# Performance work log

Hardware: AMD Instinct MI355X
Metric: run time of the kernel (lower is better)

Reference implementation:

```python
import jax, jax.numpy as jnp
import numpy as np

B, HF, WF = 16, 32, 32
DIM, NH = 1024, 16
HD = DIM // NH  # 64


def axial_freqs(H, W, head_dim):
    # RotaryEmbedding(dim=head_dim//4, freqs_for='pixel', max_freq=H*W)
    d = head_dim // 4  # rotary dim per axis
    base = jnp.linspace(1.0, (H * W) / 2.0, d // 2) * jnp.pi  # [d//2]
    posH = jnp.linspace(-1.0, 1.0, H)
    posW = jnp.linspace(-1.0, 1.0, W)
    fH = jnp.repeat(posH[:, None] * base[None, :], 2, axis=-1)  # [H, d]
    fW = jnp.repeat(posW[:, None] * base[None, :], 2, axis=-1)  # [W, d]
    fH = jnp.broadcast_to(fH[:, None, :], (H, W, d))
    fW = jnp.broadcast_to(fW[None, :, :], (H, W, d))
    return jnp.concatenate([fH, fW], axis=-1)  # [H, W, 2d] = [H, W, head_dim//2]


def rotate_half(x):
    # interleaved pair rotation: (x1, x2) -> (-x2, x1)
    xr = x.reshape(*x.shape[:-1], -1, 2)
    x1, x2 = xr[..., 0], xr[..., 1]
    return jnp.stack([-x2, x1], axis=-1).reshape(x.shape)


def apply_rotary(freqs, t):
    # t: [B, h, H, W, hd]; freqs: [H, W, rot_dim]
    rd = freqs.shape[-1]
    t_rot, t_pass = t[..., :rd], t[..., rd:]
    t_rot = t_rot * jnp.cos(freqs) + rotate_half(t_rot) * jnp.sin(freqs)
    return jnp.concatenate([t_rot, t_pass], axis=-1)


def setup_inputs() -> dict:
    key = jax.random.key(0)
    k1, k2, k3 = jax.random.split(key, 3)
    s = 1.0 / np.sqrt(DIM)
    return {
        "x": jax.random.normal(k1, (B, HF * WF, DIM), jnp.float32),
        "w_qkv": jax.random.normal(k2, (3 * DIM, DIM), jnp.float32) * s,
        "w_proj": jax.random.normal(k3, (DIM, DIM), jnp.float32) * s,
        "b_proj": jnp.zeros((DIM,), jnp.float32),
    }


def reference(x, w_qkv, w_proj, b_proj):
    freqs = axial_freqs(HF, WF, HD)
    qkv = x @ w_qkv.T  # [B, N, 3*DIM]
    q, k, v = jnp.split(qkv, 3, axis=-1)

    def to_grid(t):  # [B, N, DIM] -> [B, h, H, W, hd]
        return t.reshape(B, HF, WF, NH, HD).transpose(0, 3, 1, 2, 4)

    q, k, v = to_grid(q), to_grid(k), to_grid(v)
    q = apply_rotary(freqs, q)
    k = apply_rotary(freqs, k)
    N = HF * WF
    q = q.reshape(B, NH, N, HD)
    k = k.reshape(B, NH, N, HD)
    v = v.reshape(B, NH, N, HD)

    scale = 1.0 / np.sqrt(HD)
    attn = jax.nn.softmax(jnp.einsum('bhnd,bhmd->bhnm', q, k) * scale, axis=-1)
    out = jnp.einsum('bhnm,bhmd->bhnd', attn, v)  # [B, h, N, hd]
    out = out.transpose(0, 2, 1, 3).reshape(B, N, DIM)
    return out @ w_proj.T + b_proj
```

## Files before the change

kernel.cpp:

```cpp
#include <hip/hip_runtime.h>
#include <hip/hip_bf16.h>
#include <math.h>

typedef __bf16 bf16;
typedef bf16 bf16x4 __attribute__((ext_vector_type(4)));
typedef bf16 bf16x8 __attribute__((ext_vector_type(8)));
typedef float f32x4 __attribute__((ext_vector_type(4)));

#define MFMA16(a, b, c) __builtin_amdgcn_mfma_f32_16x16x32_bf16((a), (b), (c), 0, 0, 0)

#define QSCALE 0.18033688011112042f

__device__ __forceinline__ void async16(const void* g, void* l) {
  __builtin_amdgcn_global_load_lds(
      (const __attribute__((address_space(1))) void*)g,
      (__attribute__((address_space(3))) void*)l, 16, 0, 0);
}

__global__ __launch_bounds__(256) void f2b_all_kernel(const float* __restrict__ x,
                                                      const float* __restrict__ wqkv,
                                                      const float* __restrict__ wproj,
                                                      bf16* __restrict__ xb,
                                                      bf16* __restrict__ wqb,
                                                      bf16* __restrict__ wpb) {
  int t = blockIdx.x * 256 + threadIdx.x;
  const float* in;
  bf16* out;
  int i;
  if (t < 4194304) {
    in = x; out = xb; i = t * 4;
  } else if (t < 4980736) {
    in = wqkv; out = wqb; i = (t - 4194304) * 4;
  } else {
    in = wproj; out = wpb; i = (t - 4980736) * 4;
  }
  f32x4 v = *(const f32x4*)(in + i);
  bf16x4 o = {(bf16)v[0], (bf16)v[1], (bf16)v[2], (bf16)v[3]};
  *(bf16x4*)(out + i) = o;
}

__global__ __launch_bounds__(256) void table_kernel(float* __restrict__ cosT,
                                                    float* __restrict__ sinT) {
  int idx = blockIdx.x * 256 + threadIdx.x;
  if (idx >= 1024 * 32) return;
  int n = idx >> 5, d = idx & 31;
  int hf = n >> 5, wf = n & 31;
  int bi = (d & 15) >> 1;
  float base = (1.0f + 73.0f * bi) * 3.14159265358979323846f;
  int p = (d < 16) ? hf : wf;
  float pos = (2.0f * (float)p - 31.0f) * (1.0f / 31.0f);
  float f = pos * base;
  cosT[idx] = cosf(f);
  sinT[idx] = sinf(f);
}

template <int EPI, int NBN>
__global__ __launch_bounds__(512, 2) void gemm_bt(
    const bf16* __restrict__ A, const bf16* __restrict__ W,
    bf16* __restrict__ oq, bf16* __restrict__ okk, bf16* __restrict__ ovt,
    const float* __restrict__ cosT, const float* __restrict__ sinT,
    float* __restrict__ outF, const float* __restrict__ bias) {
  constexpr int K = 1024;
  __shared__ bf16 As[4][256 * 32];
  __shared__ bf16 Bs[4][256 * 32];

  const int tid = threadIdx.x;
  const int lane = tid & 63;
  const int wid = tid >> 6;
  const int lo = lane & 15, hi = lane >> 4;
  const int wm = wid >> 2;
  const int wn = wid & 3;

  const int wg = blockIdx.x;
  const int xcd = wg & 7;
  const int i = wg >> 3;
  const int s = i >> 4;
  const int r = i & 15;
  const int bm = xcd * 8 + (s & 1) * 4 + (r & 3);
  const int bn = (s >> 1) * 4 + (r >> 2);

  const bf16* Ab = A + (size_t)bm * 256 * K;
  const bf16* Wb = W + (size_t)bn * 256 * K;

  const f32x4 fzero = {0.f, 0.f, 0.f, 0.f};
  f32x4 acc[8][4];
#pragma unroll
  for (int i2 = 0; i2 < 8; ++i2)
#pragma unroll
    for (int j = 0; j < 4; ++j) acc[i2][j] = fzero;

  size_t srcOff[2];
  int ldsOff[2];
#pragma unroll
  for (int i2 = 0; i2 < 2; ++i2) {
    const int c = i2 * 512 + tid;
    const int row = c >> 2, g = c & 3;
    const int gsrc = g ^ ((row >> 1) & 3);
    srcOff[i2] = (size_t)row * K + gsrc * 8;
    ldsOff[i2] = c * 8;
  }

  auto stageSlot = [&](int slot, int kh) {
#pragma unroll
    for (int i2 = 0; i2 < 2; ++i2)
      async16(Ab + srcOff[i2] + kh * 32, &As[slot][ldsOff[i2]]);
#pragma unroll
    for (int i2 = 0; i2 < 2; ++i2)
      async16(Wb + srcOff[i2] + kh * 32, &Bs[slot][ldsOff[i2]]);
  };

  auto compute = [&](int slot) {
    bf16x8 af[8], bf[4];
#pragma unroll
    for (int mf = 0; mf < 8; ++mf) {
      const int row = wm * 128 + mf * 16 + lo;
      const int g = hi ^ ((row >> 1) & 3);
      af[mf] = *(const bf16x8*)&As[slot][row * 32 + g * 8];
    }
#pragma unroll
    for (int nf = 0; nf < 4; ++nf) {
      const int row = wn * 64 + nf * 16 + lo;
      const int g = hi ^ ((row >> 1) & 3);
      bf[nf] = *(const bf16x8*)&Bs[slot][row * 32 + g * 8];
    }
    __builtin_amdgcn_s_setprio(1);
#pragma unroll
    for (int mf = 0; mf < 8; ++mf)
#pragma unroll
      for (int nf = 0; nf < 4; ++nf)
        acc[mf][nf] = MFMA16(af[mf], bf[nf], acc[mf][nf]);
    __builtin_amdgcn_s_setprio(0);
  };

  stageSlot(0, 0);
  stageSlot(1, 1);

  for (int kt = 0; kt < 7; ++kt) {
#pragma unroll
    for (int ph = 0; ph < 4; ++ph) {
      stageSlot((ph + 2) & 3, kt * 4 + ph + 2);
      asm volatile("s_waitcnt vmcnt(8)" ::: "memory");
      __builtin_amdgcn_s_barrier();
      compute(ph);
    }
  }
  stageSlot(2, 30);
  asm volatile("s_waitcnt vmcnt(8)" ::: "memory");
  __builtin_amdgcn_s_barrier();
  compute(0);
  stageSlot(3, 31);
  asm volatile("s_waitcnt vmcnt(8)" ::: "memory");
  __builtin_amdgcn_s_barrier();
  compute(1);
  asm volatile("s_waitcnt vmcnt(4)" ::: "memory");
  __builtin_amdgcn_s_barrier();
  compute(2);
  asm volatile("s_waitcnt vmcnt(0)" ::: "memory");
  __builtin_amdgcn_s_barrier();
  compute(3);

  const int rb0 = bm * 256 + wm * 128;
  const int jb0 = bn * 256 + wn * 64;

  if constexpr (EPI == 0) {
#pragma unroll
    for (int ac = 0; ac < 4; ++ac) {
      const int j = jb0 + ac * 16 + lo;
      const int which = j >> 10;
      const int f = j & 1023;
      const int h = f >> 6, d = f & 63;
#pragma unroll
      for (int ar = 0; ar < 8; ++ar) {
        const int rb = rb0 + ar * 16 + 4 * hi;
        f32x4 v = acc[ar][ac];
        if (which == 2) {
          const int b = rb >> 10, n0 = rb & 1023;
          bf16x4 pk = {(bf16)v[0], (bf16)v[1], (bf16)v[2], (bf16)v[3]};
          *(bf16x4*)(ovt + ((size_t)((b * 16 + h) * 64 + d)) * 1024 + n0) = pk;
        } else {
          bf16* dst = which ? okk : oq;
          const float sc = which ? 1.0f : QSCALE;
#pragma unroll
          for (int reg = 0; reg < 4; ++reg) {
            const int r2 = rb + reg;
            const int b = r2 >> 10, n = r2 & 1023;
            float val = v[reg];
            float res;
            if (d < 32) {
              float c = cosT[n * 32 + d];
              float sn = sinT[n * 32 + d];
              float pp = __shfl_xor(val, 1);
              res = (d & 1) ? fmaf(val, c, pp * sn) : fmaf(val, c, -(pp * sn));
            } else {
              res = val;
            }
            dst[((size_t)((b * 16 + h) * 1024 + n)) * 64 + d] = (bf16)(res * sc);
          }
        }
      }
    }
  } else {
#pragma unroll
    for (int ac = 0; ac < 4; ++ac) {
      const int j = jb0 + ac * 16 + lo;
      const float bv = bias[j];
#pragma unroll
      for (int ar = 0; ar < 8; ++ar) {
        const int rb = rb0 + ar * 16 + 4 * hi;
#pragma unroll
        for (int reg = 0; reg < 4; ++reg)
          outF[(size_t)(rb + reg) * 1024 + j] = acc[ar][ac][reg] + bv;
      }
    }
  }
}

__global__ __launch_bounds__(512, 4) void attn_fwd(const bf16* __restrict__ q,
                                                   const bf16* __restrict__ k,
                                                   const bf16* __restrict__ vt,
                                                   bf16* __restrict__ o) {
  __shared__ bf16 Kt[2][64 * 64];
  __shared__ bf16 Vt[2][64 * 64];
  __shared__ bf16 Pt[8][32 * 68];
  const int tid = threadIdx.x;
  const int lane = tid & 63, wid = tid >> 6;
  const int lo = lane & 15, hi = lane >> 4;
  const int j = blockIdx.x;
  const int bh = (j & 7) + ((j >> 5) << 3);
  const int qt = (j >> 3) & 3;
  const bf16* qg = q + (size_t)bh * 65536;
  const bf16* kg = k + (size_t)bh * 65536;
  const bf16* vg = vt + (size_t)bh * 65536;

  bf16x8 qf[2][2];
#pragma unroll
  for (int rg = 0; rg < 2; ++rg) {
    const int qrow = qt * 256 + wid * 32 + rg * 16 + lo;
#pragma unroll
    for (int ch = 0; ch < 2; ++ch)
      qf[rg][ch] = *(const bf16x8*)(qg + (size_t)qrow * 64 + ch * 32 + 8 * hi);
  }

  const int srow = tid >> 3;
  const int sgsrc = (tid & 7) ^ (srow & 7);
  auto stageKV = [&](int buf, int kv) {
    async16(kg + (size_t)(kv * 64 + srow) * 64 + sgsrc * 8, &Kt[buf][tid * 8]);
    async16(vg + (size_t)srow * 1024 + kv * 64 + sgsrc * 8, &Vt[buf][tid * 8]);
  };

  asm volatile("s_waitcnt vmcnt(0)" ::: "memory");
  stageKV(0, 0);

  const f32x4 fzero = {0.f, 0.f, 0.f, 0.f};
  f32x4 of[2][4];
  float psum[2][4];
#pragma unroll
  for (int rg = 0; rg < 2; ++rg)
#pragma unroll
    for (int r = 0; r < 4; ++r) {
      of[rg][r] = fzero;
      psum[rg][r] = 0.f;
    }

  const int m7 = lo & 7;

  for (int kv = 0; kv < 16; ++kv) {
    const int cur = kv & 1;
    if (kv < 15) {
      stageKV(cur ^ 1, kv + 1);
      asm volatile("s_waitcnt vmcnt(2)" ::: "memory");
    } else {
      asm volatile("s_waitcnt vmcnt(0)" ::: "memory");
    }
    __builtin_amdgcn_s_barrier();

#pragma unroll
    for (int kf = 0; kf < 4; ++kf) {
      const int r = kf * 16 + lo;
      bf16x8 kb0 = *(const bf16x8*)&Kt[cur][r * 64 + ((hi ^ m7) * 8)];
      bf16x8 kb1 = *(const bf16x8*)&Kt[cur][r * 64 + (((hi + 4) ^ m7) * 8)];
#pragma unroll
      for (int rg = 0; rg < 2; ++rg) {
        f32x4 z = fzero;
        z = MFMA16(qf[rg][0], kb0, z);
        z = MFMA16(qf[rg][1], kb1, z);
#pragma unroll
        for (int reg = 0; reg < 4; ++reg) {
          float p = __builtin_amdgcn_exp2f(z[reg]);
          psum[rg][reg] += p;
          Pt[wid][(rg * 16 + 4 * hi + reg) * 68 + kf * 16 + lo] = (bf16)p;
        }
      }
    }

    bf16x8 pa[2][2];
#pragma unroll
    for (int rg = 0; rg < 2; ++rg)
#pragma unroll
      for (int ch = 0; ch < 2; ++ch)
        pa[rg][ch] = *(const bf16x8*)&Pt[wid][(rg * 16 + lo) * 68 + ch * 32 + 8 * hi];
#pragma unroll
    for (int df = 0; df < 4; ++df) {
      const int r = df * 16 + lo;
      bf16x8 vb0 = *(const bf16x8*)&Vt[cur][r * 64 + ((hi ^ m7) * 8)];
      bf16x8 vb1 = *(const bf16x8*)&Vt[cur][r * 64 + (((hi + 4) ^ m7) * 8)];
#pragma unroll
      for (int rg = 0; rg < 2; ++rg) {
        of[rg][df] = MFMA16(pa[rg][0], vb0, of[rg][df]);
        of[rg][df] = MFMA16(pa[rg][1], vb1, of[rg][df]);
      }
    }
    __syncthreads();
  }

#pragma unroll
  for (int off = 1; off < 16; off <<= 1) {
#pragma unroll
    for (int rg = 0; rg < 2; ++rg)
#pragma unroll
      for (int reg = 0; reg < 4; ++reg) psum[rg][reg] += __shfl_xor(psum[rg][reg], off);
  }

  const int b = bh >> 4, h = bh & 15;
#pragma unroll
  for (int rg = 0; rg < 2; ++rg)
#pragma unroll
    for (int reg = 0; reg < 4; ++reg) {
      const int n = qt * 256 + wid * 32 + rg * 16 + 4 * hi + reg;
      const float inv = 1.0f / psum[rg][reg];
#pragma unroll
      for (int df = 0; df < 4; ++df)
        o[((size_t)(b * 1024 + n)) * 1024 + h * 64 + df * 16 + lo] =
            (bf16)(of[rg][df][reg] * inv);
    }
}

extern "C" void kernel_launch(void* const* d_in, const int* in_sizes, int n_in,
                              void* d_out, int out_size, void* d_ws, size_t ws_size,
                              hipStream_t stream) {
  (void)in_sizes; (void)n_in; (void)out_size; (void)ws_size;
  const float* x = (const float*)d_in[0];
  const float* wqkv = (const float*)d_in[1];
  const float* wproj = (const float*)d_in[2];
  const float* bproj = (const float*)d_in[3];

  char* ws = (char*)d_ws;
  bf16* xb = (bf16*)(ws);
  bf16* wqb = (bf16*)(ws + 33554432);
  bf16* wpb = (bf16*)(ws + 39845888);
  float* cosT = (float*)(ws + 41943040);
  float* sinT = (float*)(ws + 42074112);
  bf16* qb = (bf16*)(ws + 42205184);
  bf16* kb = (bf16*)(ws + 75759616);
  bf16* vtb = (bf16*)(ws + 109314048);

  f2b_all_kernel<<<20480, 256, 0, stream>>>(x, wqkv, wproj, xb, wqb, wpb);
  table_kernel<<<128, 256, 0, stream>>>(cosT, sinT);

  gemm_bt<0, 12><<<768, 512, 0, stream>>>(xb, wqb, qb, kb, vtb, cosT, sinT,
                                          nullptr, nullptr);
  attn_fwd<<<1024, 512, 0, stream>>>(qb, kb, vtb, xb);
  gemm_bt<1, 4><<<256, 512, 0, stream>>>(xb, wpb, nullptr, nullptr, nullptr,
                                         nullptr, nullptr, (float*)d_out, bproj);
}
```

Baseline: 273.2 us.

## Switch attention to 32x32x16 MFMA and keep P in registers via permlane swap

```diff
diff --git a/kernel.cpp b/kernel.cpp
--- a/kernel.cpp
+++ b/kernel.cpp
@@ -3,11 +3,16 @@
 #include <math.h>
 
 typedef __bf16 bf16;
+typedef bf16 bf16x2 __attribute__((ext_vector_type(2)));
 typedef bf16 bf16x4 __attribute__((ext_vector_type(4)));
 typedef bf16 bf16x8 __attribute__((ext_vector_type(8)));
 typedef float f32x4 __attribute__((ext_vector_type(4)));
+typedef float f32x16 __attribute__((ext_vector_type(16)));
+typedef unsigned int uint;
+typedef uint uint32x4 __attribute__((ext_vector_type(4)));
 
 #define MFMA16(a, b, c) __builtin_amdgcn_mfma_f32_16x16x32_bf16((a), (b), (c), 0, 0, 0)
+#define MFMA32(a, b, c) __builtin_amdgcn_mfma_f32_32x32x16_bf16((a), (b), (c), 0, 0, 0)
 
 #define QSCALE 0.18033688011112042f
 
@@ -15,6 +20,15 @@
   __builtin_amdgcn_global_load_lds(
       (const __attribute__((address_space(1))) void*)g,
       (__attribute__((address_space(3))) void*)l, 16, 0, 0);
+}
+
+__device__ __forceinline__ uint pkbf(float a, float b) {
+  bf16x2 t = {(bf16)a, (bf16)b};
+  return __builtin_bit_cast(uint, t);
+}
+
+__device__ __forceinline__ void pls(uint& x, uint& y) {
+  asm volatile("v_permlane32_swap_b32 %0, %1" : "+v"(x), "+v"(y));
 }
 
 __global__ __launch_bounds__(256) void f2b_all_kernel(const float* __restrict__ x,
@@ -221,10 +235,12 @@
                                                    bf16* __restrict__ o) {
   __shared__ bf16 Kt[2][64 * 64];
   __shared__ bf16 Vt[2][64 * 64];
-  __shared__ bf16 Pt[8][32 * 68];
+  __shared__ float Psm[8][32];
   const int tid = threadIdx.x;
   const int lane = tid & 63, wid = tid >> 6;
-  const int lo = lane & 15, hi = lane >> 4;
+  const int l31 = lane & 31;
+  const int s = lane >> 5;
+  const int m7 = l31 & 7;
   const int j = blockIdx.x;
   const int bh = (j & 7) + ((j >> 5) << 3);
   const int qt = (j >> 3) & 3;
@@ -232,14 +248,11 @@
   const bf16* kg = k + (size_t)bh * 65536;
   const bf16* vg = vt + (size_t)bh * 65536;
 
-  bf16x8 qf[2][2];
-#pragma unroll
-  for (int rg = 0; rg < 2; ++rg) {
-    const int qrow = qt * 256 + wid * 32 + rg * 16 + lo;
-#pragma unroll
-    for (int ch = 0; ch < 2; ++ch)
-      qf[rg][ch] = *(const bf16x8*)(qg + (size_t)qrow * 64 + ch * 32 + 8 * hi);
-  }
+  const int qrow = qt * 256 + wid * 32 + l31;
+  bf16x8 qf[4];
+#pragma unroll
+  for (int kb4 = 0; kb4 < 4; ++kb4)
+    qf[kb4] = *(const bf16x8*)(qg + (size_t)qrow * 64 + kb4 * 16 + s * 8);
 
   const int srow = tid >> 3;
   const int sgsrc = (tid & 7) ^ (srow & 7);
@@ -251,18 +264,10 @@
   asm volatile("s_waitcnt vmcnt(0)" ::: "memory");
   stageKV(0, 0);
 
-  const f32x4 fzero = {0.f, 0.f, 0.f, 0.f};
-  f32x4 of[2][4];
-  float psum[2][4];
-#pragma unroll
-  for (int rg = 0; rg < 2; ++rg)
-#pragma unroll
-    for (int r = 0; r < 4; ++r) {
-      of[rg][r] = fzero;
-      psum[rg][r] = 0.f;
-    }
-
-  const int m7 = lo & 7;
+  f32x16 of0 = {0.f, 0.f, 0.f, 0.f, 0.f, 0.f, 0.f, 0.f,
+                0.f, 0.f, 0.f, 0.f, 0.f, 0.f, 0.f, 0.f};
+  f32x16 of1 = of0;
+  float psum = 0.f;
 
   for (int kv = 0; kv < 16; ++kv) {
     const int cur = kv & 1;
@@ -274,65 +279,64 @@
     }
     __builtin_amdgcn_s_barrier();
 
-#pragma unroll
-    for (int kf = 0; kf < 4; ++kf) {
-      const int r = kf * 16 + lo;
-      bf16x8 kb0 = *(const bf16x8*)&Kt[cur][r * 64 + ((hi ^ m7) * 8)];
-      bf16x8 kb1 = *(const bf16x8*)&Kt[cur][r * 64 + (((hi + 4) ^ m7) * 8)];
-#pragma unroll
-      for (int rg = 0; rg < 2; ++rg) {
-        f32x4 z = fzero;
-        z = MFMA16(qf[rg][0], kb0, z);
-        z = MFMA16(qf[rg][1], kb1, z);
-#pragma unroll
-        for (int reg = 0; reg < 4; ++reg) {
-          float p = __builtin_amdgcn_exp2f(z[reg]);
-          psum[rg][reg] += p;
-          Pt[wid][(rg * 16 + 4 * hi + reg) * 68 + kf * 16 + lo] = (bf16)p;
-        }
-      }
-    }
-
-    bf16x8 pa[2][2];
-#pragma unroll
-    for (int rg = 0; rg < 2; ++rg)
-#pragma unroll
-      for (int ch = 0; ch < 2; ++ch)
-        pa[rg][ch] = *(const bf16x8*)&Pt[wid][(rg * 16 + lo) * 68 + ch * 32 + 8 * hi];
-#pragma unroll
-    for (int df = 0; df < 4; ++df) {
-      const int r = df * 16 + lo;
-      bf16x8 vb0 = *(const bf16x8*)&Vt[cur][r * 64 + ((hi ^ m7) * 8)];
-      bf16x8 vb1 = *(const bf16x8*)&Vt[cur][r * 64 + (((hi + 4) ^ m7) * 8)];
-#pragma unroll
-      for (int rg = 0; rg < 2; ++rg) {
-        of[rg][df] = MFMA16(pa[rg][0], vb0, of[rg][df]);
-        of[rg][df] = MFMA16(pa[rg][1], vb1, of[rg][df]);
-      }
-    }
+    f32x16 z0 = {0.f, 0.f, 0.f, 0.f, 0.f, 0.f, 0.f, 0.f,
+                 0.f, 0.f, 0.f, 0.f, 0.f, 0.f, 0.f, 0.f};
+    f32x16 z1 = z0;
+#pragma unroll
+    for (int kb4 = 0; kb4 < 4; ++kb4) {
+      bf16x8 k0 = *(const bf16x8*)&Kt[cur][l31 * 64 + (((2 * kb4 + s) ^ m7) * 8)];
+      bf16x8 k1 = *(const bf16x8*)&Kt[cur][(32 + l31) * 64 + (((2 * kb4 + s) ^ m7) * 8)];
+      z0 = MFMA32(k0, qf[kb4], z0);
+      z1 = MFMA32(k1, qf[kb4], z1);
+    }
+
+    uint c0[8], c1[8];
+#pragma unroll
+    for (int m = 0; m < 8; ++m) {
+      float a0 = __builtin_amdgcn_exp2f(z0[2 * m]);
+      float b0 = __builtin_amdgcn_exp2f(z0[2 * m + 1]);
+      float a1 = __builtin_amdgcn_exp2f(z1[2 * m]);
+      float b1 = __builtin_amdgcn_exp2f(z1[2 * m + 1]);
+      psum += (a0 + b0) + (a1 + b1);
+      c0[m] = pkbf(a0, b0);
+      c1[m] = pkbf(a1, b1);
+    }
+
+    auto pv = [&](uint* cc, int bb, int kb) {
+      uint w0 = cc[4 * bb], w2 = cc[4 * bb + 2];
+      uint w1 = cc[4 * bb + 1], w3 = cc[4 * bb + 3];
+      pls(w0, w2);
+      pls(w1, w3);
+      uint32x4 W = {w0, w1, w2, w3};
+      bf16x8 apv = __builtin_bit_cast(bf16x8, W);
+      bf16x8 vb0 = *(const bf16x8*)&Vt[cur][l31 * 64 + (((2 * kb + s) ^ m7) * 8)];
+      bf16x8 vb1 = *(const bf16x8*)&Vt[cur][(32 + l31) * 64 + (((2 * kb + s) ^ m7) * 8)];
+      of0 = MFMA32(apv, vb0, of0);
+      of1 = MFMA32(apv, vb1, of1);
+    };
+    pv(c0, 0, 0);
+    pv(c0, 1, 1);
+    pv(c1, 0, 2);
+    pv(c1, 1, 3);
+
     __syncthreads();
   }
 
-#pragma unroll
-  for (int off = 1; off < 16; off <<= 1) {
-#pragma unroll
-    for (int rg = 0; rg < 2; ++rg)
-#pragma unroll
-      for (int reg = 0; reg < 4; ++reg) psum[rg][reg] += __shfl_xor(psum[rg][reg], off);
-  }
+  psum += __shfl_xor(psum, 32);
+  const float inv = 1.0f / psum;
+  if (lane < 32) Psm[wid][l31] = inv;
+  __syncthreads();
 
   const int b = bh >> 4, h = bh & 15;
 #pragma unroll
-  for (int rg = 0; rg < 2; ++rg)
-#pragma unroll
-    for (int reg = 0; reg < 4; ++reg) {
-      const int n = qt * 256 + wid * 32 + rg * 16 + 4 * hi + reg;
-      const float inv = 1.0f / psum[rg][reg];
-#pragma unroll
-      for (int df = 0; df < 4; ++df)
-        o[((size_t)(b * 1024 + n)) * 1024 + h * 64 + df * 16 + lo] =
-            (bf16)(of[rg][df][reg] * inv);
-    }
+  for (int r = 0; r < 16; ++r) {
+    const int qr = (r & 3) + 8 * (r >> 2) + 4 * s;
+    const float iv = Psm[wid][qr];
+    const int n = qt * 256 + wid * 32 + qr;
+    const size_t base = ((size_t)(b * 1024 + n)) * 1024 + h * 64 + l31;
+    o[base] = (bf16)(of0[r] * iv);
+    o[base + 32] = (bf16)(of1[r] * iv);
+  }
 }
 
 extern "C" void kernel_launch(void* const* d_in, const int* in_sizes, int n_in,
```

New measurement: 253.8 us. 7.1% less time.
